# Kernel optimization log

Measured on AMD Instinct MI355X. Metric: run time of the kernel, lower is better.

The kernel has to match this reference:

```python
import jax, jax.numpy as jnp
import numpy as np

B, T, C = 4, 2048, 2048
H, S = 32, 64
LN_EPS = 1e-5


def _layer_norm(x, w, b):
    mu = jnp.mean(x, axis=-1, keepdims=True)
    var = jnp.mean((x - mu) ** 2, axis=-1, keepdims=True)
    return (x - mu) / jnp.sqrt(var + LN_EPS) * w + b


def setup_inputs() -> dict:
    key = jax.random.key(0)
    ks = jax.random.split(key, 8)
    sc = 1.0 / np.sqrt(C)
    sc4 = 1.0 / np.sqrt(4 * C)
    return {
        "x": jax.random.normal(ks[0], (B, T, C), jnp.float32),
        "time_decay": jnp.full((H, S), -5.0, jnp.float32),
        "time_first": jnp.zeros((H, S), jnp.float32),
        "Wk": jax.random.normal(ks[1], (C, C), jnp.float32) * sc,
        "Wv": jax.random.normal(ks[2], (C, C), jnp.float32) * sc,
        "Wr": jax.random.normal(ks[3], (C, C), jnp.float32) * sc,
        "Wo": jax.random.normal(ks[4], (C, C), jnp.float32) * sc,
        "Wfk": jax.random.normal(ks[5], (C, 4 * C), jnp.float32) * sc,
        "Wfv": jax.random.normal(ks[6], (4 * C, C), jnp.float32) * sc4,
        "ln1_w": jnp.ones((C,), jnp.float32),
        "ln1_b": jnp.zeros((C,), jnp.float32),
        "ln2_w": jnp.ones((C,), jnp.float32),
        "ln2_b": jnp.zeros((C,), jnp.float32),
    }


def reference(x, time_decay, time_first, Wk, Wv, Wr, Wo, Wfk, Wfv,
              ln1_w, ln1_b, ln2_w, ln2_b):
    b, t, c = x.shape
    h, s = time_decay.shape
    xl = _layer_norm(x, ln1_w, ln1_b)
    k = (xl @ Wk).reshape(b, t, h, s)  # [B,T,H,S]
    v = (xl @ Wv).reshape(b, t, h, s)
    r = (xl @ Wr).reshape(b, t, h, s)

    decay = jnp.exp(-jnp.exp(time_decay))  # [H,S]
    u = jnp.exp(k) * v                      # [B,T,H,S]
    u_t = jnp.swapaxes(u, 0, 1)             # [T,B,H,S]

    def step(state, ut):
        state = decay * state + ut
        return state, state

    _, states = jax.lax.scan(step, jnp.zeros((b, h, s), x.dtype), u_t)  # [T,B,H,S]
    # t=0 bonus term: exp(time_first) * v_0 added to wkv only (not the state)
    states = states.at[0].add(jnp.exp(time_first) * v[:, 0])
    wkv = jnp.swapaxes(states, 0, 1)        # [B,T,H,S]

    rwkv = jax.nn.sigmoid(r) * wkv
    x = x + rwkv.reshape(b, t, c) @ Wo
    xl2 = _layer_norm(x, ln2_w, ln2_b)
    ffn = (jax.nn.relu(xl2 @ Wfk) ** 2) @ Wfv
    return x + ffn
```

## Files before the change

kernel.cpp:

```cpp
#include <hip/hip_runtime.h>
#include <hip/hip_bf16.h>
#include <stdint.h>

#define B_  4
#define T_  2048
#define C_  2048
#define H_  32
#define S_  64
#define M_  (B_ * T_)
#define C4_ (4 * C_)
#define C2_ (2 * C_)
#define LN_EPS 1e-5f
#define NCH 16
#define CLEN 128
#define NCHAN (B_ * C_)

typedef unsigned short u16;
typedef __attribute__((ext_vector_type(8))) short short8;
typedef __attribute__((ext_vector_type(4))) float f32x4;

__device__ __forceinline__ u16 f2bf(float f) {
  uint32_t u = __float_as_uint(f);
  u = (u + 0x7FFFu + ((u >> 16) & 1u)) >> 16;
  return (u16)u;
}
__device__ __forceinline__ float bf2f(u16 u) {
  return __uint_as_float(((uint32_t)u) << 16);
}

__device__ __forceinline__ void gload_lds16(const void* g, void* l) {
  __builtin_amdgcn_global_load_lds(
      (const __attribute__((address_space(1))) uint32_t*)g,
      (__attribute__((address_space(3))) uint32_t*)l, 16, 0, 0);
}

__global__ __launch_bounds__(256) void k_transpose_cast(
    const float* __restrict__ in, u16* __restrict__ out, int ld, int R, int Cn) {
  __shared__ float tile[32][33];
  const int tx = threadIdx.x & 31, ty = threadIdx.x >> 5;
  const int c0 = blockIdx.x * 32, r0 = blockIdx.y * 32;
#pragma unroll
  for (int i = 0; i < 4; ++i) {
    int r = ty + i * 8;
    tile[r][tx] = in[(size_t)(r0 + r) * ld + (c0 + tx)];
  }
  __syncthreads();
#pragma unroll
  for (int i = 0; i < 4; ++i) {
    int cc = ty + i * 8;
    out[(size_t)(c0 + cc) * R + (r0 + tx)] = f2bf(tile[tx][cc]);
  }
}

__global__ __launch_bounds__(256) void k_layernorm_bf16(
    const float* __restrict__ x, const float* __restrict__ w,
    const float* __restrict__ bias, u16* __restrict__ out) {
  const int row = blockIdx.x;
  const int t = threadIdx.x;
  const float* xr = x + (size_t)row * C_;
  float4 a = ((const float4*)xr)[2 * t];
  float4 b = ((const float4*)xr)[2 * t + 1];
  float s = a.x + a.y + a.z + a.w + b.x + b.y + b.z + b.w;
  float q = a.x * a.x + a.y * a.y + a.z * a.z + a.w * a.w +
            b.x * b.x + b.y * b.y + b.z * b.z + b.w * b.w;
#pragma unroll
  for (int off = 32; off > 0; off >>= 1) {
    s += __shfl_down(s, off);
    q += __shfl_down(q, off);
  }
  __shared__ float rs[8];
  const int wv = t >> 6;
  if ((t & 63) == 0) { rs[wv] = s; rs[4 + wv] = q; }
  __syncthreads();
  s = rs[0] + rs[1] + rs[2] + rs[3];
  q = rs[4] + rs[5] + rs[6] + rs[7];
  const float mean = s * (1.0f / C_);
  const float rstd = rsqrtf(q * (1.0f / C_) - mean * mean + LN_EPS);
  float4 w0 = ((const float4*)w)[2 * t], w1 = ((const float4*)w)[2 * t + 1];
  float4 b0 = ((const float4*)bias)[2 * t], b1 = ((const float4*)bias)[2 * t + 1];
  uint4 pk;
  pk.x = (uint32_t)f2bf((a.x - mean) * rstd * w0.x + b0.x) |
         ((uint32_t)f2bf((a.y - mean) * rstd * w0.y + b0.y) << 16);
  pk.y = (uint32_t)f2bf((a.z - mean) * rstd * w0.z + b0.z) |
         ((uint32_t)f2bf((a.w - mean) * rstd * w0.w + b0.w) << 16);
  pk.z = (uint32_t)f2bf((b.x - mean) * rstd * w1.x + b1.x) |
         ((uint32_t)f2bf((b.y - mean) * rstd * w1.y + b1.y) << 16);
  pk.w = (uint32_t)f2bf((b.z - mean) * rstd * w1.z + b1.z) |
         ((uint32_t)f2bf((b.w - mean) * rstd * w1.w + b1.w) << 16);
  ((uint4*)(out + (size_t)row * C_))[t] = pk;
}

__device__ __forceinline__ void stage_half(
    const u16* __restrict__ G, int ldK, int row0, int kcol0,
    u16* lds_half, int tid) {
#pragma unroll
  for (int i = 0; i < 2; ++i) {
    const int slot = i * 512 + tid;
    const int row = slot >> 2;
    const int gs = slot & 3;
    const int gsrc = gs ^ ((row >> 1) & 3);
    gload_lds16(G + (size_t)(row0 + row) * ldK + kcol0 + gsrc * 8,
                ((char*)lds_half) + i * 8192 + (tid >> 6) * 1024);
  }
}

__device__ __forceinline__ short8 frag(const u16* half_base, int row, int g0) {
  const int g = g0 ^ ((row >> 1) & 3);
  return *(const short8*)(half_base + row * 32 + g * 8);
}

template <int EPI>
__global__ __launch_bounds__(512, 2) void k_gemm8(
    const u16* __restrict__ A, const u16* __restrict__ Bt,
    void* __restrict__ Out, const float* __restrict__ Res,
    int M, int N, int K) {
  __shared__ u16 As[2][2][256 * 32];
  __shared__ u16 Bs[2][2][256 * 32];
  const int tid = threadIdx.x;
  const int wv = tid >> 6, ln = tid & 63;
  const int wm = wv >> 2, wn = wv & 3;
  const int l15 = ln & 15, g0 = ln >> 4;

  const int lin = blockIdx.y * gridDim.x + blockIdx.x;
  const int xcd = lin & 7, slot = lin >> 3;
  const int bx = slot % gridDim.x;
  const int by = xcd * (gridDim.y >> 3) + slot / gridDim.x;
  const int bm0 = by * 256, bn0 = bx * 256;
  const int NT = K >> 6;

  f32x4 acc[8][4];
#pragma unroll
  for (int m = 0; m < 8; ++m)
#pragma unroll
    for (int n = 0; n < 4; ++n) acc[m][n] = (f32x4)0.0f;

  stage_half(A, K, bm0, 0, &As[0][0][0], tid);
  stage_half(Bt, K, bn0, 0, &Bs[0][0][0], tid);
  stage_half(A, K, bm0, 32, &As[0][1][0], tid);
  stage_half(Bt, K, bn0, 32, &Bs[0][1][0], tid);
  asm volatile("s_waitcnt vmcnt(4)" ::: "memory");
  __builtin_amdgcn_s_barrier();

  for (int t = 0; t < NT; ++t) {
    const int c = t & 1, nb = c ^ 1;
    const int kn = (t + 1) << 6;
    const bool stage_on = (t + 1 < NT);
    const bool lastt = (t + 1 == NT);
    short8 bfr[4], af[4];

#pragma unroll
    for (int h = 0; h < 2; ++h) {
#pragma unroll
      for (int n = 0; n < 4; ++n)
        bfr[n] = frag(&Bs[c][h][0], wn * 64 + n * 16 + l15, g0);
#pragma unroll
      for (int m = 0; m < 4; ++m)
        af[m] = frag(&As[c][h][0], wm * 128 + m * 16 + l15, g0);
      if (stage_on) stage_half(A, K, bm0, kn + h * 32, &As[nb][h][0], tid);
      asm volatile("s_waitcnt lgkmcnt(0)" ::: "memory");
      __builtin_amdgcn_sched_barrier(0);
      __builtin_amdgcn_s_setprio(1);
#pragma unroll
      for (int m = 0; m < 4; ++m)
#pragma unroll
        for (int n = 0; n < 4; ++n)
          acc[m][n] = __builtin_amdgcn_mfma_f32_16x16x32_bf16(af[m], bfr[n], acc[m][n], 0, 0, 0);
      __builtin_amdgcn_s_setprio(0);

#pragma unroll
      for (int m = 0; m < 4; ++m)
        af[m] = frag(&As[c][h][0], wm * 128 + 64 + m * 16 + l15, g0);
      if (stage_on) stage_half(Bt, K, bn0, kn + h * 32, &Bs[nb][h][0], tid);
      asm volatile("s_waitcnt lgkmcnt(0)" ::: "memory");
      __builtin_amdgcn_sched_barrier(0);
      __builtin_amdgcn_s_setprio(1);
#pragma unroll
      for (int m = 0; m < 4; ++m)
#pragma unroll
        for (int n = 0; n < 4; ++n)
          acc[4 + m][n] = __builtin_amdgcn_mfma_f32_16x16x32_bf16(af[m], bfr[n], acc[4 + m][n], 0, 0, 0);
      __builtin_amdgcn_s_setprio(0);

      if (h == 0) {
        if (!lastt) asm volatile("s_waitcnt vmcnt(4)" ::: "memory");
        else        asm volatile("s_waitcnt vmcnt(0)" ::: "memory");
        __builtin_amdgcn_s_barrier();
      } else if (!lastt) {
        asm volatile("s_waitcnt vmcnt(4)" ::: "memory");
        __builtin_amdgcn_s_barrier();
      }
    }
  }

#pragma unroll
  for (int m = 0; m < 8; ++m) {
    const int r_base = bm0 + wm * 128 + m * 16 + (ln >> 4) * 4;
#pragma unroll
    for (int n = 0; n < 4; ++n) {
      const int cidx = bn0 + wn * 64 + n * 16 + l15;
#pragma unroll
      for (int i = 0; i < 4; ++i) {
        const size_t off = (size_t)(r_base + i) * N + cidx;
        const float v = acc[m][n][i];
        if constexpr (EPI == 0) {
          ((float*)Out)[off] = v;
        } else if constexpr (EPI == 1) {
          ((float*)Out)[off] = Res[off] + v;
        } else if constexpr (EPI == 2) {
          ((u16*)Out)[off] = f2bf(v);
        } else if constexpr (EPI == 3) {
          const float tpos = v > 0.0f ? v : 0.0f;
          ((u16*)Out)[off] = f2bf(tpos * tpos);
        } else {
          ((float*)Out)[off] += v;
        }
      }
    }
  }
}

__global__ __launch_bounds__(256) void k_scan_a(
    const float* __restrict__ kk, const u16* __restrict__ vv,
    const float* __restrict__ td, float* __restrict__ Sloc) {
  const int g = blockIdx.x * 256 + threadIdx.x;
  const int j = blockIdx.y;
  const int ch = g & (C_ - 1);
  const float d = __expf(-__expf(td[ch]));
  const size_t base = ((size_t)(g >> 11) * T_ + (size_t)j * CLEN) * C_ + ch;
  float s = 0.0f;
#pragma unroll 4
  for (int t = 0; t < CLEN; ++t) {
    const size_t idx = base + (size_t)t * C_;
    s = d * s + __expf(kk[idx]) * bf2f(vv[idx]);
  }
  Sloc[(size_t)j * NCHAN + g] = s;
}

__global__ __launch_bounds__(256) void k_scan_b(
    const float* __restrict__ td, const float* __restrict__ Sloc,
    float* __restrict__ carry) {
  const int g = blockIdx.x * 256 + threadIdx.x;
  const int ch = g & (C_ - 1);
  const float dL = __expf(-__expf(td[ch]) * (float)CLEN);
  float s = 0.0f;
#pragma unroll
  for (int j = 0; j < NCH; ++j) {
    carry[(size_t)j * NCHAN + g] = s;
    s = dL * s + Sloc[(size_t)j * NCHAN + g];
  }
}

__global__ __launch_bounds__(256) void k_scan_c(
    const float* __restrict__ kk, const u16* __restrict__ vv,
    const u16* __restrict__ rr, const float* __restrict__ td,
    const float* __restrict__ tf, const float* __restrict__ carry,
    u16* __restrict__ rwkv) {
  const int g = blockIdx.x * 256 + threadIdx.x;
  const int j = blockIdx.y;
  const int ch = g & (C_ - 1);
  const float d = __expf(-__expf(td[ch]));
  const float bonus = __expf(tf[ch]);
  const size_t base = ((size_t)(g >> 11) * T_ + (size_t)j * CLEN) * C_ + ch;
  float s = carry[(size_t)j * NCHAN + g];
#pragma unroll 2
  for (int t = 0; t < CLEN; ++t) {
    const size_t idx = base + (size_t)t * C_;
    const float vval = bf2f(vv[idx]);
    s = d * s + __expf(kk[idx]) * vval;
    float wkv = s;
    if (j == 0 && t == 0) wkv += bonus * vval;
    const float rv = bf2f(rr[idx]);
    const float sg = 1.0f / (1.0f + __expf(-rv));
    rwkv[idx] = f2bf(sg * wkv);
  }
}

extern "C" void kernel_launch(void* const* d_in, const int* in_sizes, int n_in,
                              void* d_out, int out_size, void* d_ws, size_t ws_size,
                              hipStream_t stream) {
  const float* x    = (const float*)d_in[0];
  const float* td   = (const float*)d_in[1];
  const float* tf   = (const float*)d_in[2];
  const float* Wk   = (const float*)d_in[3];
  const float* Wv   = (const float*)d_in[4];
  const float* Wr   = (const float*)d_in[5];
  const float* Wo   = (const float*)d_in[6];
  const float* Wfk  = (const float*)d_in[7];
  const float* Wfv  = (const float*)d_in[8];
  const float* ln1w = (const float*)d_in[9];
  const float* ln1b = (const float*)d_in[10];
  const float* ln2w = (const float*)d_in[11];
  const float* ln2b = (const float*)d_in[12];
  float* out = (float*)d_out;

  char* p = (char*)d_ws;
  auto alloc = [&](size_t bytes) {
    char* r = p;
    p += (bytes + 255) & ~(size_t)255;
    return r;
  };
  u16*   wbuf = (u16*)alloc((size_t)C_ * C_ * 2);
  u16*   xl   = (u16*)alloc((size_t)M_ * C_ * 2);
  float* kbuf = (float*)alloc((size_t)M_ * C_ * 4);
  u16*   vbuf = (u16*)alloc((size_t)M_ * C_ * 2);
  u16*   rbuf = (u16*)alloc((size_t)M_ * C_ * 2);
  float* Sloc = (float*)alloc((size_t)NCH * NCHAN * 4);
  float* carry = (float*)alloc((size_t)NCH * NCHAN * 4);
  u16* rwkv = rbuf;
  u16* hchunk = xl;
  u16* wfbuf = rbuf;

  const dim3 tgrid(C_ / 32, C_ / 32);
  const dim3 ggrid(C_ / 256, M_ / 256);

  k_layernorm_bf16<<<M_, 256, 0, stream>>>(x, ln1w, ln1b, xl);

  k_transpose_cast<<<tgrid, 256, 0, stream>>>(Wk, wbuf, C_, C_, C_);
  k_gemm8<0><<<ggrid, 512, 0, stream>>>(xl, wbuf, kbuf, nullptr, M_, C_, C_);
  k_transpose_cast<<<tgrid, 256, 0, stream>>>(Wv, wbuf, C_, C_, C_);
  k_gemm8<2><<<ggrid, 512, 0, stream>>>(xl, wbuf, vbuf, nullptr, M_, C_, C_);
  k_transpose_cast<<<tgrid, 256, 0, stream>>>(Wr, wbuf, C_, C_, C_);
  k_gemm8<2><<<ggrid, 512, 0, stream>>>(xl, wbuf, rbuf, nullptr, M_, C_, C_);

  k_scan_a<<<dim3(NCHAN / 256, NCH), 256, 0, stream>>>(kbuf, vbuf, td, Sloc);
  k_scan_b<<<dim3(NCHAN / 256), 256, 0, stream>>>(td, Sloc, carry);
  k_scan_c<<<dim3(NCHAN / 256, NCH), 256, 0, stream>>>(kbuf, vbuf, rbuf, td, tf, carry, rwkv);

  k_transpose_cast<<<tgrid, 256, 0, stream>>>(Wo, wbuf, C_, C_, C_);
  k_gemm8<1><<<ggrid, 512, 0, stream>>>(rwkv, wbuf, out, x, M_, C_, C_);

  u16* xl2 = vbuf;
  k_layernorm_bf16<<<M_, 256, 0, stream>>>(out, ln2w, ln2b, xl2);

  for (int c = 0; c < 2; ++c) {
    k_transpose_cast<<<dim3(C2_ / 32, C_ / 32), 256, 0, stream>>>(
        Wfk + (size_t)c * C2_, wfbuf, C4_, C_, C2_);
    k_gemm8<3><<<dim3(C2_ / 256, M_ / 256), 512, 0, stream>>>(
        xl2, wfbuf, hchunk, nullptr, M_, C2_, C_);
    k_transpose_cast<<<dim3(C_ / 32, C2_ / 32), 256, 0, stream>>>(
        Wfv + (size_t)c * C2_ * C_, wfbuf, C_, C2_, C_);
    k_gemm8<4><<<dim3(C_ / 256, M_ / 256), 512, 0, stream>>>(
        hchunk, wfbuf, out, nullptr, M_, C_, C2_);
  }
}
```

Measured before the change: 963.2 us.

## Add ping-pong quadrant-scheduled GEMM kernel for FFN matmuls

Adds a new bf16 MFMA GEMM kernel, k_gemm8p, that splits the 256x256 tile into four 128x128 quadrants. Each quadrant's compute is interleaved with staging one half-tile of the next K block into LDS, using explicit barriers, wait counts and priority hints. It also uses a new XOR-swizzled LDS layout for the staged halves. The two FFN GEMMs now use this kernel, and the original kernel loses its per-phase lgkmcnt waits and setprio while gaining sched_barriers after its barriers. The aim is better overlap of global-to-LDS loads with MFMA work, at the cost of more barriers and tighter scheduling constraints that could add stalls.

```diff
diff --git a/kernel.cpp b/kernel.cpp
--- a/kernel.cpp
+++ b/kernel.cpp
@@ -140,6 +140,7 @@
   stage_half(Bt, K, bn0, 32, &Bs[0][1][0], tid);
   asm volatile("s_waitcnt vmcnt(4)" ::: "memory");
   __builtin_amdgcn_s_barrier();
+  __builtin_amdgcn_sched_barrier(0);
 
   for (int t = 0; t < NT; ++t) {
     const int c = t & 1, nb = c ^ 1;
@@ -157,37 +158,31 @@
       for (int m = 0; m < 4; ++m)
         af[m] = frag(&As[c][h][0], wm * 128 + m * 16 + l15, g0);
       if (stage_on) stage_half(A, K, bm0, kn + h * 32, &As[nb][h][0], tid);
-      asm volatile("s_waitcnt lgkmcnt(0)" ::: "memory");
-      __builtin_amdgcn_sched_barrier(0);
-      __builtin_amdgcn_s_setprio(1);
 #pragma unroll
       for (int m = 0; m < 4; ++m)
 #pragma unroll
         for (int n = 0; n < 4; ++n)
           acc[m][n] = __builtin_amdgcn_mfma_f32_16x16x32_bf16(af[m], bfr[n], acc[m][n], 0, 0, 0);
-      __builtin_amdgcn_s_setprio(0);
 
 #pragma unroll
       for (int m = 0; m < 4; ++m)
         af[m] = frag(&As[c][h][0], wm * 128 + 64 + m * 16 + l15, g0);
       if (stage_on) stage_half(Bt, K, bn0, kn + h * 32, &Bs[nb][h][0], tid);
-      asm volatile("s_waitcnt lgkmcnt(0)" ::: "memory");
-      __builtin_amdgcn_sched_barrier(0);
-      __builtin_amdgcn_s_setprio(1);
 #pragma unroll
       for (int m = 0; m < 4; ++m)
 #pragma unroll
         for (int n = 0; n < 4; ++n)
           acc[4 + m][n] = __builtin_amdgcn_mfma_f32_16x16x32_bf16(af[m], bfr[n], acc[4 + m][n], 0, 0, 0);
-      __builtin_amdgcn_s_setprio(0);
 
       if (h == 0) {
         if (!lastt) asm volatile("s_waitcnt vmcnt(4)" ::: "memory");
         else        asm volatile("s_waitcnt vmcnt(0)" ::: "memory");
         __builtin_amdgcn_s_barrier();
+        __builtin_amdgcn_sched_barrier(0);
       } else if (!lastt) {
         asm volatile("s_waitcnt vmcnt(4)" ::: "memory");
         __builtin_amdgcn_s_barrier();
+        __builtin_amdgcn_sched_barrier(0);
       }
     }
   }
@@ -202,6 +197,190 @@
       for (int i = 0; i < 4; ++i) {
         const size_t off = (size_t)(r_base + i) * N + cidx;
         const float v = acc[m][n][i];
+        if constexpr (EPI == 0) {
+          ((float*)Out)[off] = v;
+        } else if constexpr (EPI == 1) {
+          ((float*)Out)[off] = Res[off] + v;
+        } else if constexpr (EPI == 2) {
+          ((u16*)Out)[off] = f2bf(v);
+        } else if constexpr (EPI == 3) {
+          const float tpos = v > 0.0f ? v : 0.0f;
+          ((u16*)Out)[off] = f2bf(tpos * tpos);
+        } else {
+          ((float*)Out)[off] += v;
+        }
+      }
+    }
+  }
+}
+
+__device__ __forceinline__ void stage_halfP(
+    const u16* __restrict__ G, int ldK, int row0, int kt0,
+    u16* half_dst, int tid) {
+#pragma unroll
+  for (int i = 0; i < 2; ++i) {
+    const int idx = i * 512 + tid;
+    const int row = idx >> 3;
+    const int p = idx & 7;
+    const int g = p ^ (row & 7);
+    gload_lds16(G + (size_t)(row0 + row) * ldK + kt0 + g * 8,
+                ((char*)half_dst) + i * 8192 + (tid >> 6) * 1024);
+  }
+}
+
+__device__ __forceinline__ short8 fragP(const u16* half_base, int lr, int kg) {
+  const int p = kg ^ (lr & 7);
+  return *(const short8*)(half_base + lr * 64 + p * 8);
+}
+
+template <int EPI>
+__global__ __launch_bounds__(512, 2) void k_gemm8p(
+    const u16* __restrict__ A, const u16* __restrict__ Bt,
+    void* __restrict__ Out, const float* __restrict__ Res,
+    int M, int N, int K) {
+  __shared__ u16 As[2][2][128 * 64];
+  __shared__ u16 Bs[2][2][128 * 64];
+  const int tid = threadIdx.x;
+  const int wv = tid >> 6, ln = tid & 63;
+  const int wm = wv >> 2, wn = wv & 3;
+  const int l15 = ln & 15, g0 = ln >> 4;
+
+  const int lin = blockIdx.y * gridDim.x + blockIdx.x;
+  const int xcd = lin & 7, slot = lin >> 3;
+  const int bx = slot % gridDim.x;
+  const int by = xcd * (gridDim.y >> 3) + slot / gridDim.x;
+  const int bm0 = by * 256, bn0 = bx * 256;
+  const int NT = K >> 6;
+
+  const int lrA = wm * 64 + l15;
+  const int lrB = wn * 32 + l15;
+
+  f32x4 acc[8][4];
+#pragma unroll
+  for (int m = 0; m < 8; ++m)
+#pragma unroll
+    for (int n = 0; n < 4; ++n) acc[m][n] = (f32x4)0.0f;
+
+  stage_halfP(A, K, bm0, 0, &As[0][0][0], tid);
+  stage_halfP(Bt, K, bn0, 0, &Bs[0][0][0], tid);
+  stage_halfP(Bt, K, bn0 + 128, 0, &Bs[0][1][0], tid);
+  stage_halfP(A, K, bm0 + 128, 0, &As[0][1][0], tid);
+  asm volatile("s_waitcnt vmcnt(4)" ::: "memory");
+  __builtin_amdgcn_s_barrier();
+  __builtin_amdgcn_sched_barrier(0);
+
+  for (int t = 0; t < NT; ++t) {
+    const int c = t & 1, nb = c ^ 1;
+    const int kn = (t + 1) << 6;
+    const bool stage_on = (t + 1 < NT);
+    short8 af0[4][2], af1[4][2], bf0[2][2], bf1[2][2];
+
+#pragma unroll
+    for (int fm = 0; fm < 4; ++fm)
+#pragma unroll
+      for (int kk = 0; kk < 2; ++kk)
+        af0[fm][kk] = fragP(&As[c][0][0], lrA + fm * 16, kk * 4 + g0);
+#pragma unroll
+    for (int fn = 0; fn < 2; ++fn)
+#pragma unroll
+      for (int kk = 0; kk < 2; ++kk)
+        bf0[fn][kk] = fragP(&Bs[c][0][0], lrB + fn * 16, kk * 4 + g0);
+    if (stage_on) stage_halfP(A, K, bm0, kn, &As[nb][0][0], tid);
+    asm volatile("s_waitcnt lgkmcnt(8)" ::: "memory");
+    __builtin_amdgcn_s_barrier();
+    asm volatile("s_waitcnt lgkmcnt(0)" ::: "memory");
+    __builtin_amdgcn_sched_barrier(0);
+    __builtin_amdgcn_s_setprio(1);
+#pragma unroll
+    for (int kk = 0; kk < 2; ++kk)
+#pragma unroll
+      for (int fm = 0; fm < 4; ++fm)
+#pragma unroll
+        for (int fn = 0; fn < 2; ++fn)
+          acc[fm][fn] = __builtin_amdgcn_mfma_f32_16x16x32_bf16(
+              af0[fm][kk], bf0[fn][kk], acc[fm][fn], 0, 0, 0);
+    __builtin_amdgcn_s_setprio(0);
+    if (stage_on) asm volatile("s_waitcnt vmcnt(4)" ::: "memory");
+    else          asm volatile("s_waitcnt vmcnt(2)" ::: "memory");
+    __builtin_amdgcn_s_barrier();
+    __builtin_amdgcn_sched_barrier(0);
+
+#pragma unroll
+    for (int fn = 0; fn < 2; ++fn)
+#pragma unroll
+      for (int kk = 0; kk < 2; ++kk)
+        bf1[fn][kk] = fragP(&Bs[c][1][0], lrB + fn * 16, kk * 4 + g0);
+    if (stage_on) stage_halfP(Bt, K, bn0, kn, &Bs[nb][0][0], tid);
+    __builtin_amdgcn_s_barrier();
+    asm volatile("s_waitcnt lgkmcnt(0)" ::: "memory");
+    __builtin_amdgcn_sched_barrier(0);
+    __builtin_amdgcn_s_setprio(1);
+#pragma unroll
+    for (int kk = 0; kk < 2; ++kk)
+#pragma unroll
+      for (int fm = 0; fm < 4; ++fm)
+#pragma unroll
+        for (int fn = 0; fn < 2; ++fn)
+          acc[fm][2 + fn] = __builtin_amdgcn_mfma_f32_16x16x32_bf16(
+              af0[fm][kk], bf1[fn][kk], acc[fm][2 + fn], 0, 0, 0);
+    __builtin_amdgcn_s_setprio(0);
+    if (stage_on) asm volatile("s_waitcnt vmcnt(4)" ::: "memory");
+    else          asm volatile("s_waitcnt vmcnt(0)" ::: "memory");
+    __builtin_amdgcn_s_barrier();
+    __builtin_amdgcn_sched_barrier(0);
+
+#pragma unroll
+    for (int fm = 0; fm < 4; ++fm)
+#pragma unroll
+      for (int kk = 0; kk < 2; ++kk)
+        af1[fm][kk] = fragP(&As[c][1][0], lrA + fm * 16, kk * 4 + g0);
+    if (stage_on) stage_halfP(Bt, K, bn0 + 128, kn, &Bs[nb][1][0], tid);
+    __builtin_amdgcn_s_barrier();
+    asm volatile("s_waitcnt lgkmcnt(0)" ::: "memory");
+    __builtin_amdgcn_sched_barrier(0);
+    __builtin_amdgcn_s_setprio(1);
+#pragma unroll
+    for (int kk = 0; kk < 2; ++kk)
+#pragma unroll
+      for (int fm = 0; fm < 4; ++fm)
+#pragma unroll
+        for (int fn = 0; fn < 2; ++fn)
+          acc[4 + fm][fn] = __builtin_amdgcn_mfma_f32_16x16x32_bf16(
+              af1[fm][kk], bf0[fn][kk], acc[4 + fm][fn], 0, 0, 0);
+    __builtin_amdgcn_s_setprio(0);
+    __builtin_amdgcn_s_barrier();
+    __builtin_amdgcn_sched_barrier(0);
+
+    if (stage_on) stage_halfP(A, K, bm0 + 128, kn, &As[nb][1][0], tid);
+    __builtin_amdgcn_s_barrier();
+    __builtin_amdgcn_sched_barrier(0);
+    __builtin_amdgcn_s_setprio(1);
+#pragma unroll
+    for (int kk = 0; kk < 2; ++kk)
+#pragma unroll
+      for (int fm = 0; fm < 4; ++fm)
+#pragma unroll
+        for (int fn = 0; fn < 2; ++fn)
+          acc[4 + fm][2 + fn] = __builtin_amdgcn_mfma_f32_16x16x32_bf16(
+              af1[fm][kk], bf1[fn][kk], acc[4 + fm][2 + fn], 0, 0, 0);
+    __builtin_amdgcn_s_setprio(0);
+    if (stage_on) {
+      asm volatile("s_waitcnt vmcnt(4)" ::: "memory");
+      __builtin_amdgcn_s_barrier();
+      __builtin_amdgcn_sched_barrier(0);
+    }
+  }
+
+#pragma unroll
+  for (int am = 0; am < 8; ++am) {
+    const int r_base = bm0 + (am >> 2) * 128 + wm * 64 + (am & 3) * 16 + g0 * 4;
+#pragma unroll
+    for (int an = 0; an < 4; ++an) {
+      const int cidx = bn0 + (an >> 1) * 128 + wn * 32 + (an & 1) * 16 + l15;
+#pragma unroll
+      for (int i = 0; i < 4; ++i) {
+        const size_t off = (size_t)(r_base + i) * N + cidx;
+        const float v = acc[am][an][i];
         if constexpr (EPI == 0) {
           ((float*)Out)[off] = v;
         } else if constexpr (EPI == 1) {
@@ -335,11 +514,11 @@
   for (int c = 0; c < 2; ++c) {
     k_transpose_cast<<<dim3(C2_ / 32, C_ / 32), 256, 0, stream>>>(
         Wfk + (size_t)c * C2_, wfbuf, C4_, C_, C2_);
-    k_gemm8<3><<<dim3(C2_ / 256, M_ / 256), 512, 0, stream>>>(
+    k_gemm8p<3><<<dim3(C2_ / 256, M_ / 256), 512, 0, stream>>>(
         xl2, wfbuf, hchunk, nullptr, M_, C2_, C_);
     k_transpose_cast<<<dim3(C_ / 32, C2_ / 32), 256, 0, stream>>>(
         Wfv + (size_t)c * C2_ * C_, wfbuf, C_, C2_, C_);
-    k_gemm8<4><<<dim3(C_ / 256, M_ / 256), 512, 0, stream>>>(
+    k_gemm8p<4><<<dim3(C_ / 256, M_ / 256), 512, 0, stream>>>(
         hchunk, wfbuf, out, nullptr, M_, C_, C2_);
   }
 }
```

Result: no change. 970.5 us (+0.8%).
